# Optimization experiments

Hardware: AMD Instinct MI355X
Metric: run time of the kernel (lower is better)

Reference implementation:

```python
import jax, jax.numpy as jnp
import numpy as np

B, L, D, H = 4, 2048, 1024, 16
DH = D // H


def setup_inputs() -> dict:
    key = jax.random.key(0)
    ks = jax.random.split(key, 8)
    scale = 1.0 / np.sqrt(D)
    q = jax.random.normal(ks[0], (B, L, D), dtype=jnp.float32)
    k = jax.random.normal(ks[1], (B, L, D), dtype=jnp.float32)
    v = jax.random.normal(ks[2], (B, L, D), dtype=jnp.float32)
    # causal mask: 1 = attend, 0 = masked (masked_fill(mask == 0, -inf))
    mask = jnp.tril(jnp.ones((L, L), dtype=bool))[None, None, :, :]
    mask = jnp.broadcast_to(mask, (B, 1, L, L))
    W_q = jax.random.normal(ks[3], (D, D), dtype=jnp.float32) * scale
    W_k = jax.random.normal(ks[4], (D, D), dtype=jnp.float32) * scale
    W_v = jax.random.normal(ks[5], (D, D), dtype=jnp.float32) * scale
    W_o = jax.random.normal(ks[6], (D, D), dtype=jnp.float32) * scale
    return {"q": q, "k": k, "v": v, "mask": mask,
            "W_q": W_q, "W_k": W_k, "W_v": W_v, "W_o": W_o}


def _split_heads(x):
    # [B, L, D] -> [B, H, L, DH]
    Bx, Lx, _ = x.shape
    return x.reshape(Bx, Lx, H, DH).transpose(0, 2, 1, 3)


def reference(q, k, v, mask, W_q, W_k, W_v, W_o):
    qh = _split_heads(q @ W_q.T)   # [B, H, L, DH]
    kh = _split_heads(k @ W_k.T)
    vh = _split_heads(v @ W_v.T)
    scores = jnp.einsum('bhqd,bhkd->bhqk', qh, kh) / np.sqrt(DH)
    scores = jnp.where(mask, scores, -jnp.inf)  # mask==0 -> -inf
    probs = jax.nn.softmax(scores, axis=-1)
    attn = jnp.einsum('bhqk,bhkd->bhqd', probs, vh)  # [B, H, L, DH]
    out = attn.transpose(0, 2, 1, 3).reshape(B, L, D)
    return out @ W_o.T
```

## Files before the change

### kernel.cpp

```cpp
#include <hip/hip_runtime.h>

typedef __attribute__((ext_vector_type(4))) float  f32x4;
typedef __attribute__((ext_vector_type(8))) short  s16x8;
typedef __attribute__((ext_vector_type(8))) unsigned short u16x8;
typedef __attribute__((ext_vector_type(4))) unsigned short u16x4;

static __device__ __forceinline__ unsigned short f2bf(float f) {
    unsigned int u = __builtin_bit_cast(unsigned int, f);
    u += 0x7fffu + ((u >> 16) & 1u);
    return (unsigned short)(u >> 16);
}

static __device__ __forceinline__ unsigned int cvt_pk_bf16(float lo, float hi) {
    unsigned int r;
    asm("v_cvt_pk_bf16_f32 %0, %1, %2" : "=v"(r) : "v"(lo), "v"(hi));
    return r;
}

static __device__ __forceinline__ void gload16(const void* g, void* l) {
    __builtin_amdgcn_global_load_lds(
        (const __attribute__((address_space(1))) void*)g,
        (__attribute__((address_space(3))) void*)l, 16, 0, 0);
}

__global__ __launch_bounds__(256)
void conv_kernel(const float* __restrict__ q, const float* __restrict__ k,
                 const float* __restrict__ v,
                 const float* __restrict__ wq, const float* __restrict__ wk,
                 const float* __restrict__ wv, const float* __restrict__ wo,
                 unsigned short* __restrict__ qb, unsigned short* __restrict__ kb,
                 unsigned short* __restrict__ vb, unsigned short* __restrict__ wb)
{
    const int bid = blockIdx.x;
    const float* src; unsigned short* dst; int inner;
    if      (bid < 4096)  { src = q;  dst = qb; inner = bid; }
    else if (bid < 8192)  { src = k;  dst = kb; inner = bid - 4096; }
    else if (bid < 12288) { src = v;  dst = vb; inner = bid - 8192; }
    else {
        const int wseg = (bid - 12288) >> 9;
        src = wseg == 0 ? wq : wseg == 1 ? wk : wseg == 2 ? wv : wo;
        dst = wb + (size_t)wseg * 1048576;
        inner = (bid - 12288) & 511;
    }
    const size_t e0 = (size_t)inner * 2048 + threadIdx.x * 8;
    f32x4 a = *(const f32x4*)(src + e0);
    f32x4 b = *(const f32x4*)(src + e0 + 4);
    u16x8 o;
    #pragma unroll
    for (int i = 0; i < 4; ++i) { o[i] = f2bf(a[i]); o[i + 4] = f2bf(b[i]); }
    *(u16x8*)(dst + e0) = o;
}

template<int EPI>
__global__ __launch_bounds__(512)
void gemm2(const unsigned short* __restrict__ A0,
           const unsigned short* __restrict__ A1,
           const unsigned short* __restrict__ A2,
           const unsigned short* __restrict__ Bw,
           unsigned short* __restrict__ O0, unsigned short* __restrict__ O1,
           unsigned short* __restrict__ O2, float* __restrict__ Of)
{
    __shared__ unsigned short Asw[2][256 * 64];
    __shared__ unsigned short Bsw[2][128 * 64];

    const int tid  = threadIdx.x;
    const int lane = tid & 63;
    const int wave = tid >> 6;
    const int wr   = wave >> 1, wc = wave & 1;
    const int g    = lane >> 4, l16 = lane & 15;

    const int nblk = (EPI == 0) ? 768 : 256;
    const int cpx  = nblk >> 3;
    const int wg   = (blockIdx.x & 7) * cpx + (blockIdx.x >> 3);
    const int bx   = wg & 7;
    const int byt  = wg >> 3;
    const int seg  = (EPI == 0) ? (byt >> 5) : 0;
    const int byl  = (EPI == 0) ? (byt & 31) : byt;

    const unsigned short* Ap = (EPI == 0) ? (seg == 0 ? A0 : seg == 1 ? A1 : A2) : A0;
    const unsigned short* Arow = Ap + (size_t)(byl * 256) * 1024;
    const unsigned short* Brow = Bw + (size_t)seg * 1048576 + (size_t)(bx * 128) * 1024;

    f32x4 acc[4][4] = {};

    auto stage = [&](int buf, int kt) {
        #pragma unroll
        for (int j = 0; j < 4; ++j) {
            const int idx = j * 512 + tid;
            const int r   = idx >> 3;
            const int cl  = (tid & 7) ^ (r & 7);
            gload16(Arow + (size_t)r * 1024 + kt * 64 + cl * 8,
                    (char*)Asw[buf] + j * 8192 + wave * 1024);
        }
        #pragma unroll
        for (int j = 0; j < 2; ++j) {
            const int idx = j * 512 + tid;
            const int r   = idx >> 3;
            const int cl  = (tid & 7) ^ (r & 7);
            gload16(Brow + (size_t)r * 1024 + kt * 64 + cl * 8,
                    (char*)Bsw[buf] + j * 8192 + wave * 1024);
        }
    };

    stage(0, 0);
    asm volatile("s_waitcnt vmcnt(0)" ::: "memory");
    __builtin_amdgcn_s_barrier();

    int cur = 0;
    for (int kt = 0; kt < 16; ++kt) {
        if (kt < 15) stage(cur ^ 1, kt + 1);

        const char* Ab = (const char*)Asw[cur];
        const char* Bb = (const char*)Bsw[cur];
        #pragma unroll
        for (int ks = 0; ks < 2; ++ks) {
            s16x8 af[4], bf[4];
            #pragma unroll
            for (int mi = 0; mi < 4; ++mi) {
                const int row = wr * 64 + mi * 16 + l16;
                const int off = (row * 128 + g * 16 + ks * 64) ^ ((row & 7) << 4);
                af[mi] = __builtin_bit_cast(s16x8, *(const u16x8*)(Ab + off));
            }
            #pragma unroll
            for (int ni = 0; ni < 4; ++ni) {
                const int row = wc * 64 + ni * 16 + l16;
                const int off = (row * 128 + g * 16 + ks * 64) ^ ((row & 7) << 4);
                bf[ni] = __builtin_bit_cast(s16x8, *(const u16x8*)(Bb + off));
            }
            #pragma unroll
            for (int mi = 0; mi < 4; ++mi)
                #pragma unroll
                for (int ni = 0; ni < 4; ++ni)
                    acc[mi][ni] = __builtin_amdgcn_mfma_f32_16x16x32_bf16(
                        af[mi], bf[ni], acc[mi][ni], 0, 0, 0);
        }

        asm volatile("s_waitcnt vmcnt(0)" ::: "memory");
        __builtin_amdgcn_s_barrier();
        cur ^= 1;
    }

    #pragma unroll
    for (int mi = 0; mi < 4; ++mi) {
        #pragma unroll
        for (int ni = 0; ni < 4; ++ni) {
            const int gr0 = byl * 256 + wr * 64 + mi * 16 + g * 4;
            const int gc  = bx * 128 + wc * 64 + ni * 16 + l16;
            if (EPI == 0 && seg == 2) {
                const int b = gr0 >> 11, ll = gr0 & 2047;
                const int h = gc >> 6,  dh = gc & 63;
                u16x4 pk;
                #pragma unroll
                for (int rr = 0; rr < 4; ++rr) pk[rr] = f2bf(acc[mi][ni][rr]);
                *(u16x4*)(O2 + (size_t)((b * 16 + h) * 64 + dh) * 2048 + ll) = pk;
            } else {
                #pragma unroll
                for (int rr = 0; rr < 4; ++rr) {
                    const int gr = gr0 + rr;
                    float v = acc[mi][ni][rr];
                    if (EPI == 0) {
                        const int b = gr >> 11, ll = gr & 2047;
                        const int h = gc >> 6,  dh = gc & 63;
                        if (seg == 0) {
                            v *= 0.125f;
                            O0[(size_t)((b * 16 + h) * 2048 + ll) * 64 + dh] = f2bf(v);
                        } else {
                            O1[(size_t)((b * 16 + h) * 2048 + ll) * 64 + dh] = f2bf(v);
                        }
                    } else {
                        Of[(size_t)gr * 1024 + gc] = v;
                    }
                }
            }
        }
    }
}

template<int AM, int BM, int EPI>
__global__ __launch_bounds__(256)
void gemm_k(const void* __restrict__ A0, const void* __restrict__ A1,
            const void* __restrict__ A2,
            const void* __restrict__ B0, const void* __restrict__ B1,
            const void* __restrict__ B2,
            unsigned short* __restrict__ O0, unsigned short* __restrict__ O1,
            unsigned short* __restrict__ O2, float* __restrict__ Of)
{
    __shared__ unsigned short Asw[128 * 64];
    __shared__ unsigned short Bsw[128 * 64];

    const int tid  = threadIdx.x;
    const int lane = tid & 63;
    const int wave = tid >> 6;
    const int wr   = wave >> 1, wc = wave & 1;
    const int g    = lane >> 4, l16 = lane & 15;

    const int nper = (EPI == 0) ? 192 : 64;
    const int wg   = (blockIdx.x & 7) * nper + (blockIdx.x >> 3);
    const int bx   = wg & 7;
    const int by   = wg >> 3;
    const int seg  = (EPI == 0) ? (by >> 6) : 0;
    const int byl  = (EPI == 0) ? (by & 63) : by;

    const void* Ap = seg == 0 ? A0 : seg == 1 ? A1 : A2;
    const void* Bp = seg == 0 ? B0 : seg == 1 ? B1 : B2;

    f32x4 acc[4][4] = {};

    for (int kt = 0; kt < 16; ++kt) {
        __syncthreads();
        if (AM == 0) {
            #pragma unroll
            for (int j = 0; j < 4; ++j) {
                const int idx = j * 256 + tid;
                const int r   = idx >> 3;
                const int cl  = (tid & 7) ^ (r & 7);
                gload16((const unsigned short*)Ap + (size_t)(byl * 128 + r) * 1024 + kt * 64 + cl * 8,
                        (char*)Asw + j * 4096 + wave * 1024);
            }
        } else {
            #pragma unroll
            for (int j = 0; j < 4; ++j) {
                const int idx = j * 256 + tid;
                const int r = idx >> 3, c = tid & 7;
                const float* src = (const float*)Ap + (size_t)(byl * 128 + r) * 1024 + kt * 64 + c * 8;
                f32x4 a = *(const f32x4*)src;
                f32x4 b = *(const f32x4*)(src + 4);
                u16x8 w;
                #pragma unroll
                for (int i = 0; i < 4; ++i) { w[i] = f2bf(a[i]); w[i + 4] = f2bf(b[i]); }
                *(u16x8*)((char*)Asw + ((r * 128 + c * 16) ^ ((r & 7) << 4))) = w;
            }
        }
        if (BM == 0) {
            #pragma unroll
            for (int j = 0; j < 4; ++j) {
                const int idx = j * 256 + tid;
                const int r   = idx >> 3;
                const int cl  = (tid & 7) ^ (r & 7);
                gload16((const unsigned short*)Bp + (size_t)(bx * 128 + r) * 1024 + kt * 64 + cl * 8,
                        (char*)Bsw + j * 4096 + wave * 1024);
            }
        } else {
            #pragma unroll
            for (int j = 0; j < 4; ++j) {
                const int idx = j * 256 + tid;
                const int r = idx >> 3, c = tid & 7;
                const float* src = (const float*)Bp + (size_t)(bx * 128 + r) * 1024 + kt * 64 + c * 8;
                f32x4 a = *(const f32x4*)src;
                f32x4 b = *(const f32x4*)(src + 4);
                u16x8 w;
                #pragma unroll
                for (int i = 0; i < 4; ++i) { w[i] = f2bf(a[i]); w[i + 4] = f2bf(b[i]); }
                *(u16x8*)((char*)Bsw + ((r * 128 + c * 16) ^ ((r & 7) << 4))) = w;
            }
        }
        __syncthreads();

        #pragma unroll
        for (int ks = 0; ks < 2; ++ks) {
            s16x8 af[4], bf[4];
            #pragma unroll
            for (int mi = 0; mi < 4; ++mi) {
                const int row = wr * 64 + mi * 16 + l16;
                const int off = (row * 128 + g * 16 + ks * 64) ^ ((row & 7) << 4);
                af[mi] = __builtin_bit_cast(s16x8, *(const u16x8*)((const char*)Asw + off));
            }
            #pragma unroll
            for (int ni = 0; ni < 4; ++ni) {
                const int row = wc * 64 + ni * 16 + l16;
                const int off = (row * 128 + g * 16 + ks * 64) ^ ((row & 7) << 4);
                bf[ni] = __builtin_bit_cast(s16x8, *(const u16x8*)((const char*)Bsw + off));
            }
            #pragma unroll
            for (int mi = 0; mi < 4; ++mi)
                #pragma unroll
                for (int ni = 0; ni < 4; ++ni)
                    acc[mi][ni] = __builtin_amdgcn_mfma_f32_16x16x32_bf16(
                        af[mi], bf[ni], acc[mi][ni], 0, 0, 0);
        }
    }

    #pragma unroll
    for (int mi = 0; mi < 4; ++mi) {
        #pragma unroll
        for (int ni = 0; ni < 4; ++ni) {
            #pragma unroll
            for (int rr = 0; rr < 4; ++rr) {
                const int gr = byl * 128 + wr * 64 + mi * 16 + g * 4 + rr;
                const int gc = bx * 128 + wc * 64 + ni * 16 + l16;
                float v = acc[mi][ni][rr];
                if (EPI == 0) {
                    const int b = gr >> 11, ll = gr & 2047, h = gc >> 6, dh = gc & 63;
                    if (seg == 0) {
                        v *= 0.125f;
                        O0[(size_t)((b * 16 + h) * 2048 + ll) * 64 + dh] = f2bf(v);
                    } else if (seg == 1) {
                        O1[(size_t)((b * 16 + h) * 2048 + ll) * 64 + dh] = f2bf(v);
                    } else {
                        O2[(size_t)((b * 16 + h) * 64 + dh) * 2048 + ll] = f2bf(v);
                    }
                } else {
                    Of[(size_t)gr * 1024 + gc] = v;
                }
            }
        }
    }
}

__global__ __launch_bounds__(512)
void attn_kernel(const unsigned short* __restrict__ Qh,
                 const unsigned short* __restrict__ Kh,
                 const unsigned short* __restrict__ Vt,
                 unsigned short* __restrict__ Ctx)
{
    __shared__ unsigned short Ksw[2][64 * 64];
    __shared__ unsigned short Vsw[2][64 * 64];
    __shared__ unsigned short Psw[8][16 * 64];

    const int tid  = threadIdx.x;
    const int lane = tid & 63;
    const int wave = tid >> 6;
    const int g    = lane >> 4, l16 = lane & 15;
    const int qb   = 15 - (int)(blockIdx.x >> 6);
    const int bh   = blockIdx.x & 63;
    const int b    = bh >> 4, h = bh & 15;
    const int qrow0 = qb * 128 + wave * 16;
    const int ntile = 2 * qb + 2;

    const int sr = tid >> 3, sc = tid & 7;
    const int soff = (sr * 128 + sc * 16) ^ ((sr & 7) << 4);
    const unsigned short* kbase = Kh + ((size_t)bh * 2048 + sr) * 64 + sc * 8;
    const unsigned short* vbase = Vt + ((size_t)bh * 64 + sr) * 2048 + sc * 8;

    s16x8 qf[2];
    {
        const unsigned short* qp = Qh + ((size_t)bh * 2048 + qrow0 + l16) * 64 + g * 8;
        qf[0] = __builtin_bit_cast(s16x8, *(const u16x8*)qp);
        qf[1] = __builtin_bit_cast(s16x8, *(const u16x8*)(qp + 32));
    }

    f32x4 o[4] = {};
    float m = -3.0e38f, l = 0.f;

    *(u16x8*)((char*)Ksw[0] + soff) = *(const u16x8*)kbase;
    *(u16x8*)((char*)Vsw[0] + soff) = *(const u16x8*)vbase;
    __syncthreads();

    int cur = 0;
    for (int t = 0; t < ntile; ++t) {
        const int kv0 = t * 64;

        u16x8 kn, vn;
        const bool hn = (t + 1 < ntile);
        if (hn) {
            kn = *(const u16x8*)(kbase + (size_t)(kv0 + 64) * 64);
            vn = *(const u16x8*)(vbase + (kv0 + 64));
        }

        if (kv0 <= qrow0 + 15) {
            const char* Kb = (const char*)Ksw[cur];
            const char* Vb = (const char*)Vsw[cur];

            f32x4 st[4] = {};
            __builtin_amdgcn_s_setprio(1);
            #pragma unroll
            for (int nt = 0; nt < 4; ++nt) {
                #pragma unroll
                for (int ks = 0; ks < 2; ++ks) {
                    const int row = nt * 16 + l16;
                    const int off = (row * 128 + g * 16 + ks * 64) ^ ((row & 7) << 4);
                    s16x8 kf = __builtin_bit_cast(s16x8, *(const u16x8*)(Kb + off));
                    st[nt] = __builtin_amdgcn_mfma_f32_16x16x32_bf16(kf, qf[ks], st[nt], 0, 0, 0);
                }
            }
            __builtin_amdgcn_s_setprio(0);

            if (kv0 + 63 > qrow0) {
                const int q_g = qrow0 + l16;
                #pragma unroll
                for (int nt = 0; nt < 4; ++nt)
                    #pragma unroll
                    for (int rr = 0; rr < 4; ++rr) {
                        const int kv_g = kv0 + nt * 16 + g * 4 + rr;
                        if (kv_g > q_g) st[nt][rr] = -3.0e38f;
                    }
            }

            float pmax = fmaxf(
                fmaxf(fmaxf(fmaxf(st[0][0], st[0][1]), fmaxf(st[0][2], st[0][3])),
                      fmaxf(fmaxf(st[1][0], st[1][1]), fmaxf(st[1][2], st[1][3]))),
                fmaxf(fmaxf(fmaxf(st[2][0], st[2][1]), fmaxf(st[2][2], st[2][3])),
                      fmaxf(fmaxf(st[3][0], st[3][1]), fmaxf(st[3][2], st[3][3]))));
            pmax = fmaxf(pmax, __shfl_xor(pmax, 16));
            pmax = fmaxf(pmax, __shfl_xor(pmax, 32));

            if (__all(pmax <= m + 8.0f)) {
                float r0 = 0.f;
                #pragma unroll
                for (int nt = 0; nt < 4; ++nt)
                    #pragma unroll
                    for (int rr = 0; rr < 4; ++rr) {
                        const float p = __expf(st[nt][rr] - m);
                        st[nt][rr] = p;
                        r0 += p;
                    }
                r0 += __shfl_xor(r0, 16);
                r0 += __shfl_xor(r0, 32);
                l += r0;
            } else {
                const float mn = fmaxf(m, pmax);
                const float scf = __expf(m - mn);
                m = mn;
                float r0 = 0.f;
                #pragma unroll
                for (int nt = 0; nt < 4; ++nt)
                    #pragma unroll
                    for (int rr = 0; rr < 4; ++rr) {
                        const float p = __expf(st[nt][rr] - mn);
                        st[nt][rr] = p;
                        r0 += p;
                    }
                r0 += __shfl_xor(r0, 16);
                r0 += __shfl_xor(r0, 32);
                l = l * scf + r0;
                float sc4[4];
                #pragma unroll
                for (int rr = 0; rr < 4; ++rr) sc4[rr] = __shfl(scf, g * 4 + rr);
                #pragma unroll
                for (int nt = 0; nt < 4; ++nt)
                    #pragma unroll
                    for (int rr = 0; rr < 4; ++rr)
                        o[nt][rr] *= sc4[rr];
            }

            unsigned short* Pw = Psw[wave];
            #pragma unroll
            for (int nt = 0; nt < 4; ++nt) {
                const unsigned int w0 = cvt_pk_bf16(st[nt][0], st[nt][1]);
                const unsigned int w1 = cvt_pk_bf16(st[nt][2], st[nt][3]);
                const int off = (l16 * 128 + nt * 32 + g * 8) ^ ((l16 & 7) << 4);
                const unsigned long long dw = ((unsigned long long)w1 << 32) | w0;
                *(unsigned long long*)((char*)Pw + off) = dw;
            }

            __builtin_amdgcn_s_setprio(1);
            #pragma unroll
            for (int ks = 0; ks < 2; ++ks) {
                const int offp = (l16 * 128 + g * 16 + ks * 64) ^ ((l16 & 7) << 4);
                s16x8 pf = __builtin_bit_cast(s16x8, *(const u16x8*)((const char*)Pw + offp));
                #pragma unroll
                for (int nt = 0; nt < 4; ++nt) {
                    const int row = nt * 16 + l16;
                    const int off = (row * 128 + g * 16 + ks * 64) ^ ((row & 7) << 4);
                    s16x8 vf = __builtin_bit_cast(s16x8, *(const u16x8*)(Vb + off));
                    o[nt] = __builtin_amdgcn_mfma_f32_16x16x32_bf16(pf, vf, o[nt], 0, 0, 0);
                }
            }
            __builtin_amdgcn_s_setprio(0);
        }

        if (hn) {
            *(u16x8*)((char*)Ksw[cur ^ 1] + soff) = kn;
            *(u16x8*)((char*)Vsw[cur ^ 1] + soff) = vn;
        }
        __syncthreads();
        cur ^= 1;
    }

    #pragma unroll
    for (int rr = 0; rr < 4; ++rr) {
        const float lq = __shfl(l, g * 4 + rr);
        const float inv = 1.0f / lq;
        const int q_g = qrow0 + g * 4 + rr;
        #pragma unroll
        for (int nt = 0; nt < 4; ++nt) {
            const int d = nt * 16 + l16;
            Ctx[((size_t)b * 2048 + q_g) * 1024 + h * 64 + d] = f2bf(o[nt][rr] * inv);
        }
    }
}

extern "C" void kernel_launch(void* const* d_in, const int* in_sizes, int n_in,
                              void* d_out, int out_size, void* d_ws, size_t ws_size,
                              hipStream_t stream)
{
    const float* q  = (const float*)d_in[0];
    const float* k  = (const float*)d_in[1];
    const float* v  = (const float*)d_in[2];
    const float* Wq = (const float*)d_in[4];
    const float* Wk = (const float*)d_in[5];
    const float* Wv = (const float*)d_in[6];
    const float* Wo = (const float*)d_in[7];

    const size_t NE = (size_t)4 * 16 * 2048 * 64;
    const size_t WE = (size_t)1024 * 1024;
    unsigned short* Qh = (unsigned short*)d_ws;
    unsigned short* Kh = Qh + NE;
    unsigned short* Vt = Kh + NE;
    float* outp = (float*)d_out;
    dim3 blk(256);

    if (ws_size >= 6 * NE * 2 + 4 * WE * 2) {
        unsigned short* qb  = Vt + NE;
        unsigned short* kb  = qb + NE;
        unsigned short* vb  = kb + NE;
        unsigned short* wb  = vb + NE;
        unsigned short* Ctx = qb;
        conv_kernel<<<dim3(14336), blk, 0, stream>>>(q, k, v, Wq, Wk, Wv, Wo,
                                                     qb, kb, vb, wb);
        gemm2<0><<<dim3(768), dim3(512), 0, stream>>>(
            qb, kb, vb, wb, Qh, Kh, Vt, nullptr);
        attn_kernel<<<dim3(1024), dim3(512), 0, stream>>>(Qh, Kh, Vt, Ctx);
        gemm2<1><<<dim3(256), dim3(512), 0, stream>>>(
            Ctx, nullptr, nullptr, wb + 3 * WE, nullptr, nullptr, nullptr, outp);
    } else {
        unsigned short* Ctx = Vt + NE;
        gemm_k<1, 1, 0><<<dim3(1536), blk, 0, stream>>>(
            q, k, v, Wq, Wk, Wv, Qh, Kh, Vt, nullptr);
        attn_kernel<<<dim3(1024), dim3(512), 0, stream>>>(Qh, Kh, Vt, Ctx);
        gemm_k<0, 1, 1><<<dim3(512), blk, 0, stream>>>(
            Ctx, nullptr, nullptr, Wo, nullptr, nullptr,
            nullptr, nullptr, nullptr, outp);
    }
}
```

Before: 200.1 us.

## Enlarge GEMM tiles to 256x256 with phased MFMA/LDS interleaving schedule

The bf16 projection GEMM now uses 256x256 output tiles with 8 waves arranged 2x4, each wave computing a 128x64 sub-tile. This halves the number of workgroups and increases operand reuse from LDS. The main loop is split into four phases that alternate LDS fragment loads with MFMA batches, separated by barriers and s_setprio, while global-to-LDS staging for the next k-tile is issued early. In exchange the kernel uses more LDS and registers and has fewer workgroups (128 for the output projection), which may underfill the CUs.

```diff
diff --git a/kernel.cpp b/kernel.cpp
--- a/kernel.cpp
+++ b/kernel.cpp
@@ -22,6 +22,15 @@
         (const __attribute__((address_space(1))) void*)g,
         (__attribute__((address_space(3))) void*)l, 16, 0, 0);
 }
+
+#define MFMA16(MB)                                                          \
+    _Pragma("unroll")                                                       \
+    for (int mi = 0; mi < 4; ++mi) {                                        \
+        _Pragma("unroll")                                                   \
+        for (int ni = 0; ni < 4; ++ni)                                      \
+            acc[(MB) + mi][ni] = __builtin_amdgcn_mfma_f32_16x16x32_bf16(   \
+                af[mi], bf[ni], acc[(MB) + mi][ni], 0, 0, 0);               \
+    }
 
 __global__ __launch_bounds__(256)
 void conv_kernel(const float* __restrict__ q, const float* __restrict__ k,
@@ -52,8 +61,8 @@
 }
 
 template<int EPI>
-__global__ __launch_bounds__(512)
-void gemm2(const unsigned short* __restrict__ A0,
+__global__ __launch_bounds__(512, 2)
+void gemmW(const unsigned short* __restrict__ A0,
            const unsigned short* __restrict__ A1,
            const unsigned short* __restrict__ A2,
            const unsigned short* __restrict__ Bw,
@@ -61,91 +70,121 @@
            unsigned short* __restrict__ O2, float* __restrict__ Of)
 {
     __shared__ unsigned short Asw[2][256 * 64];
-    __shared__ unsigned short Bsw[2][128 * 64];
+    __shared__ unsigned short Bsw[2][256 * 64];
 
     const int tid  = threadIdx.x;
     const int lane = tid & 63;
     const int wave = tid >> 6;
-    const int wr   = wave >> 1, wc = wave & 1;
+    const int wr   = wave >> 2, wc = wave & 3;
     const int g    = lane >> 4, l16 = lane & 15;
 
-    const int nblk = (EPI == 0) ? 768 : 256;
+    const int nblk = (EPI == 0) ? 384 : 128;
     const int cpx  = nblk >> 3;
     const int wg   = (blockIdx.x & 7) * cpx + (blockIdx.x >> 3);
-    const int bx   = wg & 7;
-    const int byt  = wg >> 3;
-    const int seg  = (EPI == 0) ? (byt >> 5) : 0;
-    const int byl  = (EPI == 0) ? (byt & 31) : byt;
+    const int bx   = wg & 3;
+    const int byt  = wg >> 2;
+    const int seg  = byt >> 5;
+    const int byl  = byt & 31;
 
     const unsigned short* Ap = (EPI == 0) ? (seg == 0 ? A0 : seg == 1 ? A1 : A2) : A0;
     const unsigned short* Arow = Ap + (size_t)(byl * 256) * 1024;
-    const unsigned short* Brow = Bw + (size_t)seg * 1048576 + (size_t)(bx * 128) * 1024;
-
-    f32x4 acc[4][4] = {};
-
-    auto stage = [&](int buf, int kt) {
-        #pragma unroll
-        for (int j = 0; j < 4; ++j) {
-            const int idx = j * 512 + tid;
-            const int r   = idx >> 3;
-            const int cl  = (tid & 7) ^ (r & 7);
-            gload16(Arow + (size_t)r * 1024 + kt * 64 + cl * 8,
-                    (char*)Asw[buf] + j * 8192 + wave * 1024);
-        }
-        #pragma unroll
-        for (int j = 0; j < 2; ++j) {
-            const int idx = j * 512 + tid;
-            const int r   = idx >> 3;
-            const int cl  = (tid & 7) ^ (r & 7);
-            gload16(Brow + (size_t)r * 1024 + kt * 64 + cl * 8,
-                    (char*)Bsw[buf] + j * 8192 + wave * 1024);
-        }
+    const unsigned short* Brow = Bw + (size_t)seg * 1048576 + (size_t)(bx * 256) * 1024;
+
+    f32x4 acc[8][4] = {};
+
+    auto stageA = [&](int buf, int kt2, int j) {
+        const int idx = j * 512 + tid;
+        const int r   = idx >> 3;
+        const int cl  = (tid & 7) ^ (r & 7);
+        gload16(Arow + (size_t)r * 1024 + kt2 * 64 + cl * 8,
+                (char*)Asw[buf] + j * 8192 + wave * 1024);
     };
-
-    stage(0, 0);
+    auto stageB = [&](int buf, int kt2, int j) {
+        const int idx = j * 512 + tid;
+        const int r   = idx >> 3;
+        const int cl  = (tid & 7) ^ (r & 7);
+        gload16(Brow + (size_t)r * 1024 + kt2 * 64 + cl * 8,
+                (char*)Bsw[buf] + j * 8192 + wave * 1024);
+    };
+    auto lda = [&](const char* Ab, int mi, int ks) -> s16x8 {
+        const int row = wr * 128 + mi * 16 + l16;
+        const int off = (row * 128 + g * 16 + ks * 64) ^ ((row & 7) << 4);
+        return __builtin_bit_cast(s16x8, *(const u16x8*)(Ab + off));
+    };
+    auto ldb = [&](const char* Bb, int ni, int ks) -> s16x8 {
+        const int row = wc * 64 + ni * 16 + l16;
+        const int off = (row * 128 + g * 16 + ks * 64) ^ ((row & 7) << 4);
+        return __builtin_bit_cast(s16x8, *(const u16x8*)(Bb + off));
+    };
+
+    #pragma unroll
+    for (int j = 0; j < 4; ++j) stageA(0, 0, j);
+    #pragma unroll
+    for (int j = 0; j < 4; ++j) stageB(0, 0, j);
     asm volatile("s_waitcnt vmcnt(0)" ::: "memory");
     __builtin_amdgcn_s_barrier();
 
-    int cur = 0;
-    for (int kt = 0; kt < 16; ++kt) {
-        if (kt < 15) stage(cur ^ 1, kt + 1);
-
+    for (int t = 0; t < 16; ++t) {
+        const int cur = t & 1;
         const char* Ab = (const char*)Asw[cur];
         const char* Bb = (const char*)Bsw[cur];
-        #pragma unroll
-        for (int ks = 0; ks < 2; ++ks) {
-            s16x8 af[4], bf[4];
-            #pragma unroll
-            for (int mi = 0; mi < 4; ++mi) {
-                const int row = wr * 64 + mi * 16 + l16;
-                const int off = (row * 128 + g * 16 + ks * 64) ^ ((row & 7) << 4);
-                af[mi] = __builtin_bit_cast(s16x8, *(const u16x8*)(Ab + off));
-            }
-            #pragma unroll
-            for (int ni = 0; ni < 4; ++ni) {
-                const int row = wc * 64 + ni * 16 + l16;
-                const int off = (row * 128 + g * 16 + ks * 64) ^ ((row & 7) << 4);
-                bf[ni] = __builtin_bit_cast(s16x8, *(const u16x8*)(Bb + off));
-            }
-            #pragma unroll
-            for (int mi = 0; mi < 4; ++mi)
-                #pragma unroll
-                for (int ni = 0; ni < 4; ++ni)
-                    acc[mi][ni] = __builtin_amdgcn_mfma_f32_16x16x32_bf16(
-                        af[mi], bf[ni], acc[mi][ni], 0, 0, 0);
-        }
-
+        s16x8 af[4], bf[4];
+
+        #pragma unroll
+        for (int ni = 0; ni < 4; ++ni) bf[ni] = ldb(Bb, ni, 0);
+        #pragma unroll
+        for (int mi = 0; mi < 4; ++mi) af[mi] = lda(Ab, mi, 0);
+        if (t + 1 < 16) {
+            const int nb = cur ^ 1;
+            #pragma unroll
+            for (int j = 0; j < 4; ++j) stageA(nb, t + 1, j);
+            #pragma unroll
+            for (int j = 0; j < 4; ++j) stageB(nb, t + 1, j);
+        }
+        __builtin_amdgcn_s_barrier();
+        asm volatile("s_waitcnt lgkmcnt(0)" ::: "memory");
+        __builtin_amdgcn_s_setprio(1);
+        MFMA16(0)
+        __builtin_amdgcn_s_setprio(0);
+        __builtin_amdgcn_s_barrier();
+
+        #pragma unroll
+        for (int mi = 0; mi < 4; ++mi) af[mi] = lda(Ab, 4 + mi, 0);
+        __builtin_amdgcn_s_barrier();
+        asm volatile("s_waitcnt lgkmcnt(0)" ::: "memory");
+        __builtin_amdgcn_s_setprio(1);
+        MFMA16(4)
+        __builtin_amdgcn_s_setprio(0);
+        __builtin_amdgcn_s_barrier();
+
+        #pragma unroll
+        for (int ni = 0; ni < 4; ++ni) bf[ni] = ldb(Bb, ni, 1);
+        #pragma unroll
+        for (int mi = 0; mi < 4; ++mi) af[mi] = lda(Ab, mi, 1);
+        __builtin_amdgcn_s_barrier();
+        asm volatile("s_waitcnt lgkmcnt(0)" ::: "memory");
+        __builtin_amdgcn_s_setprio(1);
+        MFMA16(0)
+        __builtin_amdgcn_s_setprio(0);
+        __builtin_amdgcn_s_barrier();
+
+        #pragma unroll
+        for (int mi = 0; mi < 4; ++mi) af[mi] = lda(Ab, 4 + mi, 1);
+        __builtin_amdgcn_s_barrier();
+        asm volatile("s_waitcnt lgkmcnt(0)" ::: "memory");
+        __builtin_amdgcn_s_setprio(1);
+        MFMA16(4)
+        __builtin_amdgcn_s_setprio(0);
         asm volatile("s_waitcnt vmcnt(0)" ::: "memory");
         __builtin_amdgcn_s_barrier();
-        cur ^= 1;
     }
 
     #pragma unroll
-    for (int mi = 0; mi < 4; ++mi) {
+    for (int mi = 0; mi < 8; ++mi) {
         #pragma unroll
         for (int ni = 0; ni < 4; ++ni) {
-            const int gr0 = byl * 256 + wr * 64 + mi * 16 + g * 4;
-            const int gc  = bx * 128 + wc * 64 + ni * 16 + l16;
+            const int gr0 = byl * 256 + wr * 128 + mi * 16 + g * 4;
+            const int gc  = bx * 256 + wc * 64 + ni * 16 + l16;
             if (EPI == 0 && seg == 2) {
                 const int b = gr0 >> 11, ll = gr0 & 2047;
                 const int h = gc >> 6,  dh = gc & 63;
@@ -508,10 +547,10 @@
         unsigned short* Ctx = qb;
         conv_kernel<<<dim3(14336), blk, 0, stream>>>(q, k, v, Wq, Wk, Wv, Wo,
                                                      qb, kb, vb, wb);
-        gemm2<0><<<dim3(768), dim3(512), 0, stream>>>(
+        gemmW<0><<<dim3(384), dim3(512), 0, stream>>>(
             qb, kb, vb, wb, Qh, Kh, Vt, nullptr);
         attn_kernel<<<dim3(1024), dim3(512), 0, stream>>>(Qh, Kh, Vt, Ctx);
-        gemm2<1><<<dim3(256), dim3(512), 0, stream>>>(
+        gemmW<1><<<dim3(128), dim3(512), 0, stream>>>(
             Ctx, nullptr, nullptr, wb + 3 * WE, nullptr, nullptr, nullptr, outp);
     } else {
         unsigned short* Ctx = Vt + NE;
```

Measured after the change: 207.7 us. 1.04x slower.

## Replace LDS-staged GEMM with register-direct global loads and smaller tiles

Applied to the files above, without the earlier changes.

The projection GEMMs no longer stage A and B tiles through double-buffered shared memory. Each wave now loads its MFMA fragments straight from global memory into registers, ping-ponging between two register sets, and uses s_setprio around the MFMA bursts. The block tile shrinks from 256x128 to 128x128 with 256 threads, so twice as many blocks launch and more fit per CU. This removes LDS traffic and barriers, but it gives up cross-wave data reuse: every wave re-reads its rows from global memory and L2 through 16-byte strided loads.

```diff
diff --git a/kernel.cpp b/kernel.cpp
--- a/kernel.cpp
+++ b/kernel.cpp
@@ -52,99 +52,76 @@
 }
 
 template<int EPI>
-__global__ __launch_bounds__(512)
-void gemm2(const unsigned short* __restrict__ A0,
+__global__ __launch_bounds__(256, 3)
+void gemmR(const unsigned short* __restrict__ A0,
            const unsigned short* __restrict__ A1,
            const unsigned short* __restrict__ A2,
            const unsigned short* __restrict__ Bw,
            unsigned short* __restrict__ O0, unsigned short* __restrict__ O1,
            unsigned short* __restrict__ O2, float* __restrict__ Of)
 {
-    __shared__ unsigned short Asw[2][256 * 64];
-    __shared__ unsigned short Bsw[2][128 * 64];
-
     const int tid  = threadIdx.x;
     const int lane = tid & 63;
     const int wave = tid >> 6;
     const int wr   = wave >> 1, wc = wave & 1;
     const int g    = lane >> 4, l16 = lane & 15;
 
-    const int nblk = (EPI == 0) ? 768 : 256;
+    const int nblk = (EPI == 0) ? 1536 : 512;
     const int cpx  = nblk >> 3;
     const int wg   = (blockIdx.x & 7) * cpx + (blockIdx.x >> 3);
     const int bx   = wg & 7;
     const int byt  = wg >> 3;
-    const int seg  = (EPI == 0) ? (byt >> 5) : 0;
-    const int byl  = (EPI == 0) ? (byt & 31) : byt;
+    const int seg  = (EPI == 0) ? (byt >> 6) : 0;
+    const int byl  = (EPI == 0) ? (byt & 63) : byt;
 
     const unsigned short* Ap = (EPI == 0) ? (seg == 0 ? A0 : seg == 1 ? A1 : A2) : A0;
-    const unsigned short* Arow = Ap + (size_t)(byl * 256) * 1024;
-    const unsigned short* Brow = Bw + (size_t)seg * 1048576 + (size_t)(bx * 128) * 1024;
+    const unsigned short* Abase = Ap + (size_t)(byl * 128 + wr * 64 + l16) * 1024 + g * 8;
+    const unsigned short* Bbase = Bw + (size_t)seg * 1048576
+                                + (size_t)(bx * 128 + wc * 64 + l16) * 1024 + g * 8;
 
     f32x4 acc[4][4] = {};
-
-    auto stage = [&](int buf, int kt) {
-        #pragma unroll
-        for (int j = 0; j < 4; ++j) {
-            const int idx = j * 512 + tid;
-            const int r   = idx >> 3;
-            const int cl  = (tid & 7) ^ (r & 7);
-            gload16(Arow + (size_t)r * 1024 + kt * 64 + cl * 8,
-                    (char*)Asw[buf] + j * 8192 + wave * 1024);
-        }
-        #pragma unroll
-        for (int j = 0; j < 2; ++j) {
-            const int idx = j * 512 + tid;
-            const int r   = idx >> 3;
-            const int cl  = (tid & 7) ^ (r & 7);
-            gload16(Brow + (size_t)r * 1024 + kt * 64 + cl * 8,
-                    (char*)Bsw[buf] + j * 8192 + wave * 1024);
-        }
-    };
-
-    stage(0, 0);
-    asm volatile("s_waitcnt vmcnt(0)" ::: "memory");
-    __builtin_amdgcn_s_barrier();
-
-    int cur = 0;
-    for (int kt = 0; kt < 16; ++kt) {
-        if (kt < 15) stage(cur ^ 1, kt + 1);
-
-        const char* Ab = (const char*)Asw[cur];
-        const char* Bb = (const char*)Bsw[cur];
-        #pragma unroll
-        for (int ks = 0; ks < 2; ++ks) {
-            s16x8 af[4], bf[4];
-            #pragma unroll
-            for (int mi = 0; mi < 4; ++mi) {
-                const int row = wr * 64 + mi * 16 + l16;
-                const int off = (row * 128 + g * 16 + ks * 64) ^ ((row & 7) << 4);
-                af[mi] = __builtin_bit_cast(s16x8, *(const u16x8*)(Ab + off));
-            }
-            #pragma unroll
-            for (int ni = 0; ni < 4; ++ni) {
-                const int row = wc * 64 + ni * 16 + l16;
-                const int off = (row * 128 + g * 16 + ks * 64) ^ ((row & 7) << 4);
-                bf[ni] = __builtin_bit_cast(s16x8, *(const u16x8*)(Bb + off));
-            }
-            #pragma unroll
-            for (int mi = 0; mi < 4; ++mi)
-                #pragma unroll
-                for (int ni = 0; ni < 4; ++ni)
-                    acc[mi][ni] = __builtin_amdgcn_mfma_f32_16x16x32_bf16(
-                        af[mi], bf[ni], acc[mi][ni], 0, 0, 0);
-        }
-
-        asm volatile("s_waitcnt vmcnt(0)" ::: "memory");
-        __builtin_amdgcn_s_barrier();
-        cur ^= 1;
-    }
+    s16x8 aA[4], bA[4], aB[4], bB[4];
+
+#define LOADF(AF, BF, KT)                                                          \
+    {                                                                              \
+        _Pragma("unroll")                                                          \
+        for (int mi = 0; mi < 4; ++mi)                                             \
+            AF[mi] = __builtin_bit_cast(s16x8,                                     \
+                *(const u16x8*)(Abase + (size_t)mi * 16384 + (KT) * 32));          \
+        _Pragma("unroll")                                                          \
+        for (int ni = 0; ni < 4; ++ni)                                             \
+            BF[ni] = __builtin_bit_cast(s16x8,                                     \
+                *(const u16x8*)(Bbase + (size_t)ni * 16384 + (KT) * 32));          \
+    }
+
+#define MFMAR(AF, BF)                                                              \
+    {                                                                              \
+        __builtin_amdgcn_s_setprio(1);                                             \
+        _Pragma("unroll")                                                          \
+        for (int mi = 0; mi < 4; ++mi) {                                           \
+            _Pragma("unroll")                                                      \
+            for (int ni = 0; ni < 4; ++ni)                                         \
+                acc[mi][ni] = __builtin_amdgcn_mfma_f32_16x16x32_bf16(             \
+                    AF[mi], BF[ni], acc[mi][ni], 0, 0, 0);                         \
+        }                                                                          \
+        __builtin_amdgcn_s_setprio(0);                                             \
+    }
+
+    LOADF(aA, bA, 0)
+    for (int kt = 0; kt < 32; kt += 2) {
+        LOADF(aB, bB, kt + 1)
+        MFMAR(aA, bA)
+        if (kt + 2 < 32) LOADF(aA, bA, kt + 2)
+        MFMAR(aB, bB)
+    }
+#undef LOADF
+#undef MFMAR
 
     #pragma unroll
     for (int mi = 0; mi < 4; ++mi) {
         #pragma unroll
         for (int ni = 0; ni < 4; ++ni) {
-            const int gr0 = byl * 256 + wr * 64 + mi * 16 + g * 4;
+            const int gr0 = byl * 128 + wr * 64 + mi * 16 + g * 4;
             const int gc  = bx * 128 + wc * 64 + ni * 16 + l16;
             if (EPI == 0 && seg == 2) {
                 const int b = gr0 >> 11, ll = gr0 & 2047;
@@ -508,10 +485,10 @@
         unsigned short* Ctx = qb;
         conv_kernel<<<dim3(14336), blk, 0, stream>>>(q, k, v, Wq, Wk, Wv, Wo,
                                                      qb, kb, vb, wb);
-        gemm2<0><<<dim3(768), dim3(512), 0, stream>>>(
+        gemmR<0><<<dim3(1536), blk, 0, stream>>>(
             qb, kb, vb, wb, Qh, Kh, Vt, nullptr);
         attn_kernel<<<dim3(1024), dim3(512), 0, stream>>>(Qh, Kh, Vt, Ctx);
-        gemm2<1><<<dim3(256), dim3(512), 0, stream>>>(
+        gemmR<1><<<dim3(512), blk, 0, stream>>>(
             Ctx, nullptr, nullptr, wb + 3 * WE, nullptr, nullptr, nullptr, outp);
     } else {
         unsigned short* Ctx = Vt + NE;
```

After: 326.5 us. +63.2%, slower.
